# Performance work log

Hardware: AMD Instinct MI355X
Metric: run time of the kernel (lower is better)

## Reference

```python
import math
import jax, jax.numpy as jnp
import numpy as np

B, LA, LB, H = 16, 1024, 1024, 512
NEG = -10000000.0


def setup_inputs() -> dict:
    key = jax.random.key(0)
    k1, k2, k3, k4 = jax.random.split(key, 4)
    a = jax.random.normal(k1, (B, LA, H), dtype=jnp.float32)
    b = jax.random.normal(k2, (B, LB, H), dtype=jnp.float32)
    mask_a = jax.random.randint(k3, (B, LA, 1), 0, 2, dtype=jnp.int32)
    mask_b = jax.random.randint(k4, (B, LB, 1), 0, 2, dtype=jnp.int32)
    temperature = jnp.asarray(1.0 / math.sqrt(H), dtype=jnp.float32)
    return {"a": a, "b": b, "mask_a": mask_a, "mask_b": mask_b, "temperature": temperature}


def reference(a, b, mask_a, mask_b, temperature):
    # attn[b,i,j] = <a_i, b_j> * temperature  -> [B, LA, LB]
    attn = jnp.einsum("bid,bjd->bij", a, b) * temperature
    # pairwise validity mask: outer product of per-token masks
    mask = jnp.einsum("bik,bjk->bij", mask_a.astype(jnp.float32), mask_b.astype(jnp.float32)) > 0
    attn = jnp.where(mask, attn, NEG)
    attn_a = jax.nn.softmax(attn, axis=1)  # softmax over a-tokens
    attn_b = jax.nn.softmax(attn, axis=2)  # softmax over b-tokens
    feature_b = jnp.einsum("bij,bid->bjd", attn_a, a)  # [B, LB, H]
    feature_a = jnp.einsum("bij,bjd->bid", attn_b, b)  # [B, LA, H]
    return (feature_a, feature_b)
```

## Files before the change

kernel.cpp:

```cpp
#include <hip/hip_runtime.h>
#include <hip/hip_bf16.h>

#define NB_ 16
#define LA_ 1024
#define LB_ 1024
#define H_  512

typedef __attribute__((ext_vector_type(8))) short short8;
typedef __attribute__((ext_vector_type(4))) float f32x4;

using bf16 = __hip_bfloat16;

__device__ __forceinline__ float bf2f(unsigned short u) {
    union { unsigned int i; float f; } c; c.i = ((unsigned)u) << 16; return c.f;
}
__device__ __forceinline__ unsigned short f2bf(float f) {
    bf16 h = __float2bfloat16(f);
    return *(unsigned short*)&h;
}

__device__ __forceinline__ void load_lds16(const void* g, void* l) {
    __builtin_amdgcn_global_load_lds(
        (const __attribute__((address_space(1))) void*)g,
        (__attribute__((address_space(3))) void*)l, 16, 0, 0);
}

__device__ __forceinline__ void gemm_core64(
    const unsigned short* __restrict__ A, const unsigned short* __restrict__ B,
    int lda, int ldb, int K,
    unsigned short* ldsA, unsigned short* ldsB, f32x4 acc[4][4])
{
    const int t = threadIdx.x;
    const int wave = t >> 6, lane = t & 63;
    const int wr = wave >> 1, wc = wave & 1;
    const int lm = lane & 15, q = lane >> 4;

    int aoff[4], boff[4];
#pragma unroll
    for (int f = 0; f < 4; f++) {
        const int ra = wr * 64 + f * 16 + lm;
        aoff[f] = ra * 128 + ((q ^ (ra & 7)) << 4);
        const int rb = wc * 64 + f * 16 + lm;
        boff[f] = rb * 128 + ((q ^ (rb & 7)) << 4);
    }

    const int row0 = wave * 8 + (lane >> 3);
    const int sc = (lane & 7) ^ (row0 & 7);
    const unsigned short* gA0 = A + (size_t)row0 * lda + sc * 8;
    const unsigned short* gB0 = B + (size_t)row0 * ldb + sc * 8;
    const int sA = 32 * lda, sB = 32 * ldb;
    char* lA = (char*)ldsA + wave * 1024;
    char* lB = (char*)ldsB + wave * 1024;

    for (int k0 = 0; k0 < K; k0 += 64) {
        __syncthreads();
#pragma unroll
        for (int s = 0; s < 4; s++) {
            load_lds16(gA0 + k0 + s * sA, lA + s * 4096);
            load_lds16(gB0 + k0 + s * sB, lB + s * 4096);
        }
        __syncthreads();
#pragma unroll
        for (int kk = 0; kk < 2; kk++) {
            const int kx = kk << 6;
            short8 av[4];
#pragma unroll
            for (int fm = 0; fm < 4; fm++)
                av[fm] = *(const short8*)((const char*)ldsA + (aoff[fm] ^ kx));
#pragma unroll
            for (int fn = 0; fn < 4; fn++) {
                const short8 bv = *(const short8*)((const char*)ldsB + (boff[fn] ^ kx));
#pragma unroll
                for (int fm = 0; fm < 4; fm++)
                    acc[fm][fn] = __builtin_amdgcn_mfma_f32_16x16x32_bf16(
                        av[fm], bv, acc[fm][fn], 0, 0, 0);
            }
        }
    }
}

__global__ __launch_bounds__(256) void k_gemm_attn(
    const unsigned short* __restrict__ a_bf, const unsigned short* __restrict__ b_bf,
    const int* __restrict__ mask_a, const int* __restrict__ mask_b,
    const float* __restrict__ temp_p,
    unsigned short* __restrict__ E, unsigned short* __restrict__ ET,
    float* __restrict__ l_row, float* __restrict__ l_col)
{
    __shared__ unsigned short lds[16384];
    unsigned short* ldsA = lds;
    unsigned short* ldsB = lds + 8192;

    const int g = blockIdx.x;
    const int batch = g & 15;
    const int qq = g >> 4;
    const int i0 = (qq >> 3) * 128, j0 = (qq & 7) * 128;

    const unsigned short* A = a_bf + (size_t)batch * LA_ * H_ + (size_t)i0 * H_;
    const unsigned short* B = b_bf + (size_t)batch * LB_ * H_ + (size_t)j0 * H_;
    f32x4 acc[4][4];
#pragma unroll
    for (int x = 0; x < 4; x++)
#pragma unroll
        for (int y = 0; y < 4; y++) acc[x][y] = 0;

    gemm_core64(A, B, H_, H_, H_, ldsA, ldsB, acc);

    const float temp = temp_p[0];
    const int t = threadIdx.x, wave = t >> 6, lane = t & 63;
    const int wr = wave >> 1, wc = wave & 1, lm = lane & 15, q = lane >> 4;
    const int* map = mask_a + batch * LA_;
    const int* mbp = mask_b + batch * LB_;
    unsigned short* Ep  = E  + (size_t)batch * LA_ * LB_;
    unsigned short* ETp = ET + (size_t)batch * LB_ * LA_;
    float* lrp = l_row + batch * LA_;
    float* lcp = l_col + batch * LB_;

    int mb[4];
#pragma unroll
    for (int fn = 0; fn < 4; fn++) mb[fn] = mbp[j0 + wc * 64 + fn * 16 + lm];

#pragma unroll
    for (int fm = 0; fm < 4; fm++) {
        const int ib = i0 + wr * 64 + fm * 16 + q * 4;
        int ma[4];
#pragma unroll
        for (int r = 0; r < 4; r++) ma[r] = map[ib + r];
#pragma unroll
        for (int fn = 0; fn < 4; fn++) {
            const int j = j0 + wc * 64 + fn * 16 + lm;
            ushort4 pk;
            unsigned short* pp = (unsigned short*)&pk;
#pragma unroll
            for (int r = 0; r < 4; r++) {
                const float e = (ma[r] && mb[fn]) ? __expf(acc[fm][fn][r] * temp) : 0.0f;
                acc[fm][fn][r] = e;
                pp[r] = f2bf(e);
            }
            *(ushort4*)(ETp + (size_t)j * LA_ + ib) = pk;
        }
    }

#pragma unroll
    for (int fm = 0; fm < 4; fm++)
#pragma unroll
        for (int r = 0; r < 4; r++) {
            float s = acc[fm][0][r] + acc[fm][1][r] + acc[fm][2][r] + acc[fm][3][r];
            s += __shfl_xor(s, 1, 16); s += __shfl_xor(s, 2, 16);
            s += __shfl_xor(s, 4, 16); s += __shfl_xor(s, 8, 16);
            if (lm == 0) atomicAdd(&lrp[i0 + wr * 64 + fm * 16 + q * 4 + r], s);
        }
#pragma unroll
    for (int fn = 0; fn < 4; fn++) {
        float s = 0.0f;
#pragma unroll
        for (int fm = 0; fm < 4; fm++)
#pragma unroll
            for (int r = 0; r < 4; r++) s += acc[fm][fn][r];
        s += __shfl_xor(s, 16, 64); s += __shfl_xor(s, 32, 64);
        if (lane < 16) atomicAdd(&lcp[j0 + wc * 64 + fn * 16 + lm], s);
    }

    __syncthreads();
#pragma unroll
    for (int fm = 0; fm < 4; fm++)
#pragma unroll
        for (int fn = 0; fn < 4; fn++)
#pragma unroll
            for (int r = 0; r < 4; r++) {
                const int il = wr * 64 + fm * 16 + q * 4 + r;
                const int jl = wc * 64 + fn * 16 + lm;
                lds[il * 128 + (((jl >> 3) ^ ((il >> 1) & 7)) << 3) + (jl & 7)] =
                    f2bf(acc[fm][fn][r]);
            }
    __syncthreads();
#pragma unroll
    for (int rep = 0; rep < 8; rep++) {
        const int il = (t >> 4) + rep * 16;
        const int jc = t & 15;
        const int phys = jc ^ ((il >> 1) & 7);
        short8 v = *(const short8*)(lds + il * 128 + phys * 8);
        *(short8*)(Ep + (size_t)(i0 + il) * LB_ + j0 + jc * 8) = v;
    }
}

__global__ __launch_bounds__(256) void k_gemm_feat(
    const unsigned short* __restrict__ E, const unsigned short* __restrict__ ET,
    const unsigned short* __restrict__ aT, const unsigned short* __restrict__ bT,
    const int* __restrict__ mask_a, const int* __restrict__ mask_b,
    const int* __restrict__ nA, const int* __restrict__ nB,
    const float* __restrict__ l_row, const float* __restrict__ l_col,
    const float* __restrict__ mean_a, const float* __restrict__ mean_b,
    float* __restrict__ out)
{
    __shared__ unsigned short lds[16384];
    unsigned short* ldsA = lds;
    unsigned short* ldsB = lds + 8192;

    const int g = blockIdx.x;
    const int zc = g & 31;
    const int qq = g >> 5;
    const int n0 = (qq & 3) * 128, m0 = (qq >> 2) * 128;

    const int batch = zc & 15;
    const bool isA = zc < 16;
    const unsigned short* Amat = (isA ? E : ET) + (size_t)batch * 1024 * 1024;
    const unsigned short* Bm   = (isA ? bT : aT) + (size_t)batch * H_ * 1024;
    const int* mp   = (isA ? mask_a : mask_b) + batch * 1024;
    const int nn    = (isA ? nB : nA)[batch];
    const float* sp = (isA ? l_row : l_col) + batch * 1024;
    const float* mv = (isA ? mean_b : mean_a) + batch * H_;
    float* op = out + (isA ? (size_t)0 : (size_t)NB_ * LA_ * H_) + (size_t)batch * 1024 * H_;

    f32x4 acc[4][4];
#pragma unroll
    for (int x = 0; x < 4; x++)
#pragma unroll
        for (int y = 0; y < 4; y++) acc[x][y] = 0;

    gemm_core64(Amat + (size_t)m0 * 1024, Bm + (size_t)n0 * 1024,
                1024, 1024, 1024, ldsA, ldsB, acc);

    const int t = threadIdx.x, wave = t >> 6, lane = t & 63;
    const int wr = wave >> 1, wc = wave & 1, lm = lane & 15, q = lane >> 4;

    float mval[4];
#pragma unroll
    for (int fn = 0; fn < 4; fn++) mval[fn] = mv[n0 + wc * 64 + fn * 16 + lm];

#pragma unroll
    for (int fm = 0; fm < 4; fm++) {
        const int ib = m0 + wr * 64 + fm * 16 + q * 4;
#pragma unroll
        for (int r = 0; r < 4; r++) {
            const int i = ib + r;
            const bool valid = (mp[i] != 0) && (nn > 0);
            const float inv = valid ? 1.0f / sp[i] : 0.0f;
#pragma unroll
            for (int fn = 0; fn < 4; fn++) {
                const int d = n0 + wc * 64 + fn * 16 + lm;
                op[(size_t)i * H_ + d] = valid ? acc[fm][fn][r] * inv : mval[fn];
            }
        }
    }
}

__global__ __launch_bounds__(256) void k_prep(
    const float* __restrict__ a, const float* __restrict__ b,
    unsigned short* __restrict__ aN, unsigned short* __restrict__ bN,
    unsigned short* __restrict__ aT, unsigned short* __restrict__ bT,
    float* __restrict__ mean_a, float* __restrict__ mean_b)
{
    __shared__ unsigned short lds[64][68];
    __shared__ float smean[64];
    const int z = blockIdx.z;
    const int batch = z & 15, sel = z >> 4;
    const float* src = sel ? b : a;
    unsigned short* np = (sel ? bN : aN) + (size_t)batch * 1024 * H_;
    unsigned short* tp = (sel ? bT : aT) + (size_t)batch * H_ * 1024;
    float* mdst = (sel ? mean_b : mean_a) + batch * H_;
    const float* sp = src + (size_t)batch * 1024 * H_;

    const int d0 = blockIdx.x * 64, i0 = blockIdx.y * 64;
    const int t = threadIdx.x;
    if (t < 64) smean[t] = 0.0f;
    const int c4 = (t & 15) * 4;
#pragma unroll
    for (int it = 0; it < 4; it++) {
        const int r = (t >> 4) + it * 16;
        float4 v = *(const float4*)(sp + (size_t)(i0 + r) * H_ + d0 + c4);
        ushort4 u = make_ushort4(f2bf(v.x), f2bf(v.y), f2bf(v.z), f2bf(v.w));
        *(ushort4*)(np + (size_t)(i0 + r) * H_ + d0 + c4) = u;
        *(ushort4*)&lds[r][c4] = u;
    }
    __syncthreads();
#pragma unroll
    for (int it = 0; it < 4; it++) {
        const int dd = (t >> 4) + it * 16;
        const int i4 = (t & 15) * 4;
        ushort4 u = make_ushort4(lds[i4][dd], lds[i4 + 1][dd], lds[i4 + 2][dd], lds[i4 + 3][dd]);
        *(ushort4*)(tp + (size_t)(d0 + dd) * 1024 + i0 + i4) = u;
        atomicAdd(&smean[dd], bf2f(u.x) + bf2f(u.y) + bf2f(u.z) + bf2f(u.w));
    }
    __syncthreads();
    if (t < 64) atomicAdd(&mdst[d0 + t], smean[t] * (1.0f / 1024.0f));
}

__global__ __launch_bounds__(256) void k_init(
    float* __restrict__ accum_zero,
    const int* __restrict__ mask_a, const int* __restrict__ mask_b,
    int* __restrict__ nA, int* __restrict__ nB)
{
    const int g = blockIdx.x, t = threadIdx.x;
    if (g < 48) {
        *(float4*)(accum_zero + (size_t)(g * 256 + t) * 4) = make_float4(0, 0, 0, 0);
        return;
    }
    const int sel = g - 48;
    const int batch = sel & 15, which = sel >> 4;
    const int* m = (which ? mask_b : mask_a) + batch * 1024;
    int s = m[t] + m[t + 256] + m[t + 512] + m[t + 768];
    __shared__ int red[256];
    red[t] = s;
    __syncthreads();
    for (int off = 128; off; off >>= 1) {
        if (t < off) red[t] += red[t + off];
        __syncthreads();
    }
    if (t == 0) (which ? nB : nA)[batch] = red[0];
}

extern "C" void kernel_launch(void* const* d_in, const int* in_sizes, int n_in,
                              void* d_out, int out_size, void* d_ws, size_t ws_size,
                              hipStream_t stream)
{
    const float* a      = (const float*)d_in[0];
    const float* b      = (const float*)d_in[1];
    const int*   mask_a = (const int*)d_in[2];
    const int*   mask_b = (const int*)d_in[3];
    const float* temp   = (const float*)d_in[4];
    float* out = (float*)d_out;

    char* ws = (char*)d_ws;
    size_t off = 0;
    unsigned short* E    = (unsigned short*)(ws + off); off += (size_t)NB_ * LA_ * LB_ * 2;
    unsigned short* ET   = (unsigned short*)(ws + off); off += (size_t)NB_ * LB_ * LA_ * 2;
    unsigned short* a_bf = (unsigned short*)(ws + off); off += (size_t)NB_ * LA_ * H_ * 2;
    unsigned short* b_bf = (unsigned short*)(ws + off); off += (size_t)NB_ * LB_ * H_ * 2;
    unsigned short* aT   = (unsigned short*)(ws + off); off += (size_t)NB_ * H_ * LA_ * 2;
    unsigned short* bT   = (unsigned short*)(ws + off); off += (size_t)NB_ * H_ * LB_ * 2;
    float* l_row  = (float*)(ws + off); off += (size_t)NB_ * LA_ * 4;
    float* l_col  = (float*)(ws + off); off += (size_t)NB_ * LB_ * 4;
    float* mean_a = (float*)(ws + off); off += (size_t)NB_ * H_ * 4;
    float* mean_b = (float*)(ws + off); off += (size_t)NB_ * H_ * 4;
    int*   nA     = (int*)(ws + off); off += 64;
    int*   nB     = (int*)(ws + off); off += 64;

    k_init<<<dim3(80), 256, 0, stream>>>(l_row, mask_a, mask_b, nA, nB);

    k_prep<<<dim3(H_ / 64, 1024 / 64, 32), 256, 0, stream>>>(
        a, b, a_bf, b_bf, aT, bT, mean_a, mean_b);

    k_gemm_attn<<<dim3(1024), 256, 0, stream>>>(
        a_bf, b_bf, mask_a, mask_b, temp, E, ET, l_row, l_col);

    k_gemm_feat<<<dim3(1024), 256, 0, stream>>>(
        E, ET, aT, bT, mask_a, mask_b, nA, nB, l_row, l_col, mean_a, mean_b, out);
}
```

Before: 228.6 us.

## Use 256x256 tiles with 8 waves and double-buffered LDS prefetch in GEMMs

Replaces the 128x128, 4-wave GEMM core with a 256x256, 8-wave core that double-buffers 64-wide K slices in 128KB of LDS. The next slice is prefetched while the current one is consumed, and MFMA issue is wrapped in barriers with raised priority. This is meant to cut redundant global re-reads and hide load latency behind compute. The attention epilogue now writes E into the LDS transpose buffer during the exp pass, which removes a separate pass. In exchange the grid shrinks to 256 blocks with one block per CU, raising register and LDS pressure and lowering occupancy.

```diff
diff --git a/kernel.cpp b/kernel.cpp
--- a/kernel.cpp
+++ b/kernel.cpp
@@ -25,89 +25,120 @@
         (__attribute__((address_space(3))) void*)l, 16, 0, 0);
 }
 
-__device__ __forceinline__ void gemm_core64(
+__device__ __forceinline__ void gemm_core256(
     const unsigned short* __restrict__ A, const unsigned short* __restrict__ B,
     int lda, int ldb, int K,
-    unsigned short* ldsA, unsigned short* ldsB, f32x4 acc[4][4])
+    unsigned short* lds, f32x4 acc[8][4])
 {
     const int t = threadIdx.x;
-    const int wave = t >> 6, lane = t & 63;
-    const int wr = wave >> 1, wc = wave & 1;
+    const int w = t >> 6, lane = t & 63;
+    const int wr = w >> 2, wc = w & 3;
     const int lm = lane & 15, q = lane >> 4;
 
-    int aoff[4], boff[4];
+    int aoff[8], boff[4];
+#pragma unroll
+    for (int f = 0; f < 8; f++) {
+        const int ra = wr * 128 + f * 16 + lm;
+        aoff[f] = ra * 128 + ((q ^ (ra & 7)) << 4);
+    }
 #pragma unroll
     for (int f = 0; f < 4; f++) {
-        const int ra = wr * 64 + f * 16 + lm;
-        aoff[f] = ra * 128 + ((q ^ (ra & 7)) << 4);
         const int rb = wc * 64 + f * 16 + lm;
         boff[f] = rb * 128 + ((q ^ (rb & 7)) << 4);
     }
 
-    const int row0 = wave * 8 + (lane >> 3);
-    const int sc = (lane & 7) ^ (row0 & 7);
-    const unsigned short* gA0 = A + (size_t)row0 * lda + sc * 8;
-    const unsigned short* gB0 = B + (size_t)row0 * ldb + sc * 8;
-    const int sA = 32 * lda, sB = 32 * ldb;
-    char* lA = (char*)ldsA + wave * 1024;
-    char* lB = (char*)ldsB + wave * 1024;
-
-    for (int k0 = 0; k0 < K; k0 += 64) {
-        __syncthreads();
-#pragma unroll
-        for (int s = 0; s < 4; s++) {
-            load_lds16(gA0 + k0 + s * sA, lA + s * 4096);
-            load_lds16(gB0 + k0 + s * sB, lB + s * 4096);
+    const int rstep = w * 8 + (lane >> 3);
+    const int sc = (lane & 7) ^ (lane >> 3);
+    const unsigned short* gA = A + (size_t)rstep * lda + sc * 8;
+    const unsigned short* gB = B + (size_t)rstep * ldb + sc * 8;
+    char* lA = (char*)lds + w * 1024;
+    char* lB = (char*)lds + 65536 + w * 1024;
+    const int NT = K >> 6;
+
+#pragma unroll
+    for (int s = 0; s < 4; s++) {
+        load_lds16(gA + (size_t)s * 64 * lda, lA + s * 8192);
+        load_lds16(gB + (size_t)s * 64 * ldb, lB + s * 8192);
+    }
+    __syncthreads();
+
+    int db = 0;
+    for (int kt = 0; kt < NT; ++kt) {
+        const char* bA = (const char*)lds + db * 32768;
+        const char* bB = (const char*)lds + 65536 + db * 32768;
+        const int nxt = (db ^ 1) * 32768;
+        short8 av[4][2];
+#pragma unroll
+        for (int p = 0; p < 4; ++p) {
+            const int pm = p >> 1, pn = p & 1;
+            if (p == 0 && kt + 1 < NT) {
+                const size_t ko = (size_t)(kt + 1) * 64;
+#pragma unroll
+                for (int s = 0; s < 4; s++) {
+                    load_lds16(gA + ko + (size_t)s * 64 * lda, lA + nxt + s * 8192);
+                    load_lds16(gB + ko + (size_t)s * 64 * ldb, lB + nxt + s * 8192);
+                }
+            }
+            if (pn == 0) {
+#pragma unroll
+                for (int f = 0; f < 4; f++)
+#pragma unroll
+                    for (int kk = 0; kk < 2; kk++)
+                        av[f][kk] = *(const short8*)(bA + (aoff[pm * 4 + f] ^ (kk << 6)));
+            }
+            short8 bv[2][2];
+#pragma unroll
+            for (int f = 0; f < 2; f++)
+#pragma unroll
+                for (int kk = 0; kk < 2; kk++)
+                    bv[f][kk] = *(const short8*)(bB + (boff[pn * 2 + f] ^ (kk << 6)));
+            __builtin_amdgcn_s_barrier();
+            __builtin_amdgcn_s_setprio(1);
+#pragma unroll
+            for (int kk = 0; kk < 2; kk++)
+#pragma unroll
+                for (int f = 0; f < 2; f++)
+#pragma unroll
+                    for (int m = 0; m < 4; m++)
+                        acc[pm * 4 + m][pn * 2 + f] =
+                            __builtin_amdgcn_mfma_f32_16x16x32_bf16(
+                                av[m][kk], bv[f][kk],
+                                acc[pm * 4 + m][pn * 2 + f], 0, 0, 0);
+            __builtin_amdgcn_s_setprio(0);
+            if (p < 3) __builtin_amdgcn_s_barrier();
         }
         __syncthreads();
-#pragma unroll
-        for (int kk = 0; kk < 2; kk++) {
-            const int kx = kk << 6;
-            short8 av[4];
-#pragma unroll
-            for (int fm = 0; fm < 4; fm++)
-                av[fm] = *(const short8*)((const char*)ldsA + (aoff[fm] ^ kx));
-#pragma unroll
-            for (int fn = 0; fn < 4; fn++) {
-                const short8 bv = *(const short8*)((const char*)ldsB + (boff[fn] ^ kx));
-#pragma unroll
-                for (int fm = 0; fm < 4; fm++)
-                    acc[fm][fn] = __builtin_amdgcn_mfma_f32_16x16x32_bf16(
-                        av[fm], bv, acc[fm][fn], 0, 0, 0);
-            }
-        }
-    }
-}
-
-__global__ __launch_bounds__(256) void k_gemm_attn(
+        db ^= 1;
+    }
+}
+
+__global__ __launch_bounds__(512, 2) void k_gemm_attn(
     const unsigned short* __restrict__ a_bf, const unsigned short* __restrict__ b_bf,
     const int* __restrict__ mask_a, const int* __restrict__ mask_b,
     const float* __restrict__ temp_p,
     unsigned short* __restrict__ E, unsigned short* __restrict__ ET,
     float* __restrict__ l_row, float* __restrict__ l_col)
 {
-    __shared__ unsigned short lds[16384];
-    unsigned short* ldsA = lds;
-    unsigned short* ldsB = lds + 8192;
+    __shared__ unsigned short lds[65536];
 
     const int g = blockIdx.x;
     const int batch = g & 15;
     const int qq = g >> 4;
-    const int i0 = (qq >> 3) * 128, j0 = (qq & 7) * 128;
+    const int i0 = (qq >> 2) * 256, j0 = (qq & 3) * 256;
 
     const unsigned short* A = a_bf + (size_t)batch * LA_ * H_ + (size_t)i0 * H_;
     const unsigned short* B = b_bf + (size_t)batch * LB_ * H_ + (size_t)j0 * H_;
-    f32x4 acc[4][4];
-#pragma unroll
-    for (int x = 0; x < 4; x++)
+    f32x4 acc[8][4];
+#pragma unroll
+    for (int x = 0; x < 8; x++)
 #pragma unroll
         for (int y = 0; y < 4; y++) acc[x][y] = 0;
 
-    gemm_core64(A, B, H_, H_, H_, ldsA, ldsB, acc);
+    gemm_core256(A, B, H_, H_, H_, lds, acc);
 
     const float temp = temp_p[0];
-    const int t = threadIdx.x, wave = t >> 6, lane = t & 63;
-    const int wr = wave >> 1, wc = wave & 1, lm = lane & 15, q = lane >> 4;
+    const int t = threadIdx.x, w = t >> 6, lane = t & 63;
+    const int wr = w >> 2, wc = w & 3, lm = lane & 15, q = lane >> 4;
     const int* map = mask_a + batch * LA_;
     const int* mbp = mask_b + batch * LB_;
     unsigned short* Ep  = E  + (size_t)batch * LA_ * LB_;
@@ -115,45 +146,47 @@
     float* lrp = l_row + batch * LA_;
     float* lcp = l_col + batch * LB_;
 
-    int mb[4];
-#pragma unroll
-    for (int fn = 0; fn < 4; fn++) mb[fn] = mbp[j0 + wc * 64 + fn * 16 + lm];
-
-#pragma unroll
-    for (int fm = 0; fm < 4; fm++) {
-        const int ib = i0 + wr * 64 + fm * 16 + q * 4;
+    int mb4[4];
+#pragma unroll
+    for (int fn = 0; fn < 4; fn++) mb4[fn] = mbp[j0 + wc * 64 + fn * 16 + lm];
+
+#pragma unroll
+    for (int fm = 0; fm < 8; fm++) {
+        const int ilb = wr * 128 + fm * 16 + q * 4;
         int ma[4];
 #pragma unroll
-        for (int r = 0; r < 4; r++) ma[r] = map[ib + r];
+        for (int r = 0; r < 4; r++) ma[r] = map[i0 + ilb + r];
 #pragma unroll
         for (int fn = 0; fn < 4; fn++) {
-            const int j = j0 + wc * 64 + fn * 16 + lm;
+            const int jl = wc * 64 + fn * 16 + lm;
             ushort4 pk;
             unsigned short* pp = (unsigned short*)&pk;
 #pragma unroll
             for (int r = 0; r < 4; r++) {
-                const float e = (ma[r] && mb[fn]) ? __expf(acc[fm][fn][r] * temp) : 0.0f;
+                const float e = (ma[r] && mb4[fn]) ? __expf(acc[fm][fn][r] * temp) : 0.0f;
                 acc[fm][fn][r] = e;
                 pp[r] = f2bf(e);
+                const int il = ilb + r;
+                lds[il * 256 + ((((jl >> 3) ^ ((il >> 1) & 15)) << 3) | (jl & 7))] = pp[r];
             }
-            *(ushort4*)(ETp + (size_t)j * LA_ + ib) = pk;
+            *(ushort4*)(ETp + (size_t)(j0 + jl) * LA_ + i0 + ilb) = pk;
         }
     }
 
 #pragma unroll
-    for (int fm = 0; fm < 4; fm++)
+    for (int fm = 0; fm < 8; fm++)
 #pragma unroll
         for (int r = 0; r < 4; r++) {
             float s = acc[fm][0][r] + acc[fm][1][r] + acc[fm][2][r] + acc[fm][3][r];
             s += __shfl_xor(s, 1, 16); s += __shfl_xor(s, 2, 16);
             s += __shfl_xor(s, 4, 16); s += __shfl_xor(s, 8, 16);
-            if (lm == 0) atomicAdd(&lrp[i0 + wr * 64 + fm * 16 + q * 4 + r], s);
+            if (lm == 0) atomicAdd(&lrp[i0 + wr * 128 + fm * 16 + q * 4 + r], s);
         }
 #pragma unroll
     for (int fn = 0; fn < 4; fn++) {
         float s = 0.0f;
 #pragma unroll
-        for (int fm = 0; fm < 4; fm++)
+        for (int fm = 0; fm < 8; fm++)
 #pragma unroll
             for (int r = 0; r < 4; r++) s += acc[fm][fn][r];
         s += __shfl_xor(s, 16, 64); s += __shfl_xor(s, 32, 64);
@@ -162,28 +195,16 @@
 
     __syncthreads();
 #pragma unroll
-    for (int fm = 0; fm < 4; fm++)
-#pragma unroll
-        for (int fn = 0; fn < 4; fn++)
-#pragma unroll
-            for (int r = 0; r < 4; r++) {
-                const int il = wr * 64 + fm * 16 + q * 4 + r;
-                const int jl = wc * 64 + fn * 16 + lm;
-                lds[il * 128 + (((jl >> 3) ^ ((il >> 1) & 7)) << 3) + (jl & 7)] =
-                    f2bf(acc[fm][fn][r]);
-            }
-    __syncthreads();
-#pragma unroll
-    for (int rep = 0; rep < 8; rep++) {
-        const int il = (t >> 4) + rep * 16;
-        const int jc = t & 15;
-        const int phys = jc ^ ((il >> 1) & 7);
-        short8 v = *(const short8*)(lds + il * 128 + phys * 8);
-        *(short8*)(Ep + (size_t)(i0 + il) * LB_ + j0 + jc * 8) = v;
-    }
-}
-
-__global__ __launch_bounds__(256) void k_gemm_feat(
+    for (int rep = 0; rep < 16; rep++) {
+        const int il = (t >> 5) + rep * 16;
+        const int c = t & 31;
+        const int phys = c ^ ((il >> 1) & 15);
+        short8 v = *(const short8*)(lds + il * 256 + phys * 8);
+        *(short8*)(Ep + (size_t)(i0 + il) * LB_ + j0 + c * 8) = v;
+    }
+}
+
+__global__ __launch_bounds__(512, 2) void k_gemm_feat(
     const unsigned short* __restrict__ E, const unsigned short* __restrict__ ET,
     const unsigned short* __restrict__ aT, const unsigned short* __restrict__ bT,
     const int* __restrict__ mask_a, const int* __restrict__ mask_b,
@@ -192,14 +213,12 @@
     const float* __restrict__ mean_a, const float* __restrict__ mean_b,
     float* __restrict__ out)
 {
-    __shared__ unsigned short lds[16384];
-    unsigned short* ldsA = lds;
-    unsigned short* ldsB = lds + 8192;
+    __shared__ unsigned short lds[65536];
 
     const int g = blockIdx.x;
     const int zc = g & 31;
     const int qq = g >> 5;
-    const int n0 = (qq & 3) * 128, m0 = (qq >> 2) * 128;
+    const int n0 = (qq & 1) * 256, m0 = (qq >> 1) * 256;
 
     const int batch = zc & 15;
     const bool isA = zc < 16;
@@ -211,25 +230,25 @@
     const float* mv = (isA ? mean_b : mean_a) + batch * H_;
     float* op = out + (isA ? (size_t)0 : (size_t)NB_ * LA_ * H_) + (size_t)batch * 1024 * H_;
 
-    f32x4 acc[4][4];
-#pragma unroll
-    for (int x = 0; x < 4; x++)
+    f32x4 acc[8][4];
+#pragma unroll
+    for (int x = 0; x < 8; x++)
 #pragma unroll
         for (int y = 0; y < 4; y++) acc[x][y] = 0;
 
-    gemm_core64(Amat + (size_t)m0 * 1024, Bm + (size_t)n0 * 1024,
-                1024, 1024, 1024, ldsA, ldsB, acc);
-
-    const int t = threadIdx.x, wave = t >> 6, lane = t & 63;
-    const int wr = wave >> 1, wc = wave & 1, lm = lane & 15, q = lane >> 4;
+    gemm_core256(Amat + (size_t)m0 * 1024, Bm + (size_t)n0 * 1024,
+                 1024, 1024, 1024, lds, acc);
+
+    const int t = threadIdx.x, w = t >> 6, lane = t & 63;
+    const int wr = w >> 2, wc = w & 3, lm = lane & 15, q = lane >> 4;
 
     float mval[4];
 #pragma unroll
     for (int fn = 0; fn < 4; fn++) mval[fn] = mv[n0 + wc * 64 + fn * 16 + lm];
 
 #pragma unroll
-    for (int fm = 0; fm < 4; fm++) {
-        const int ib = m0 + wr * 64 + fm * 16 + q * 4;
+    for (int fm = 0; fm < 8; fm++) {
+        const int ib = m0 + wr * 128 + fm * 16 + q * 4;
 #pragma unroll
         for (int r = 0; r < 4; r++) {
             const int i = ib + r;
@@ -340,9 +359,9 @@
     k_prep<<<dim3(H_ / 64, 1024 / 64, 32), 256, 0, stream>>>(
         a, b, a_bf, b_bf, aT, bT, mean_a, mean_b);
 
-    k_gemm_attn<<<dim3(1024), 256, 0, stream>>>(
+    k_gemm_attn<<<dim3(256), 512, 0, stream>>>(
         a_bf, b_bf, mask_a, mask_b, temp, E, ET, l_row, l_col);
 
-    k_gemm_feat<<<dim3(1024), 256, 0, stream>>>(
+    k_gemm_feat<<<dim3(256), 512, 0, stream>>>(
         E, ET, aT, bT, mask_a, mask_b, nA, nB, l_row, l_col, mean_a, mean_b, out);
 }
```

After: 220.2 us. 1.04x faster.
